# Kernel tuning notes

Measured on AMD Instinct MI355X. Metric: run time of the kernel, lower is better.

The kernel has to match this reference:

```python
import jax, jax.numpy as jnp
import numpy as np

# __init__ constants
COORS_RANGE = ((-51.2, 51.2), (-51.2, 51.2), (-4.0, 2.4))  # x, y, z ranges
SPATIAL = (512, 512, 64)  # base spatial shape (X, Y, Z)
SCALES = (2, 4, 8, 1)     # scale_list + [1]
N_POINTS = 2_000_000
N_BATCH = 8


def setup_inputs() -> dict:
    key = jax.random.key(0)
    kp, kb = jax.random.split(key)
    lo = jnp.array([r[0] for r in COORS_RANGE], dtype=jnp.float32)
    hi = jnp.array([r[1] for r in COORS_RANGE], dtype=jnp.float32)
    u = jax.random.uniform(kp, (N_POINTS, 3), dtype=jnp.float32)
    points = lo + u * (hi - lo)  # [N,3] xyz inside the voxelization range
    batch_idx = jax.random.randint(kb, (N_POINTS,), 0, N_BATCH).astype(jnp.int64)
    return {"points": points, "batch_idx": batch_idx}


def reference(points, batch_idx):
    """Per scale: quantize xyz to voxel indices, then unique/dedup with inverse and
    counts. Rows [b,x,y,z] are packed into a single int64 key so that a 1-D unique
    (lexicographically equivalent to torch.unique(dim=0)) can be used.
    Returns, for each scale in SCALES: (full_coors [N,4] int64, coors_inv [N] int,
    coors [M,4] int32 in [b,z,y,x] order), flattened into one tuple."""
    b = batch_idx.astype(jnp.int64)
    outs = []
    for scale in SCALES:
        dims = [int(np.ceil(s / scale)) for s in SPATIAL]  # per-scale grid size
        idxs = []
        for i in range(3):
            lo, hi = COORS_RANGE[i]
            # torch .long() truncates toward zero; values are >=0 in range so
            # truncation == floor here.
            idxs.append((dims[i] * (points[:, i] - lo) / (hi - lo)).astype(jnp.int64))
        xidx, yidx, zidx = idxs
        full_coors = jnp.stack([b, xidx, yidx, zidx], axis=-1)  # [N,4]
        sx, sy, sz = dims
        # pack (b,x,y,z) lexicographically into one key
        keys = ((b * sx + xidx) * sy + yidx) * sz + zidx
        unq, unq_inv, unq_cnt = jnp.unique(keys, return_inverse=True, return_counts=True)
        zb = unq % sz
        rem = unq // sz
        yb = rem % sy
        rem = rem // sy
        xb = rem % sx
        bb = rem // sx
        # original reorders unq columns to [b, z, y, x] and casts to int32
        coors = jnp.stack([bb, zb, yb, xb], axis=-1).astype(jnp.int32)
        outs.extend([full_coors, unq_inv.reshape(-1), coors])
    return tuple(outs)
```

## Files before the change

### kernel.cpp

```cpp
#include <hip/hip_runtime.h>
#include <stdint.h>


#define CHUNK 4096
#define NB    1174
#define TOTALW 4808704
#define R_S2 0
#define R_S4 528384
#define R_S8 598016
#define R_S1 610304

__device__ __forceinline__ uint32_t cmp2(uint32_t w) {
  w = (w | (w >> 1)) & 0x55555555u;
  w = (w | (w >> 1)) & 0x33333333u;
  w = (w | (w >> 2)) & 0x0F0F0F0Fu;
  w = (w | (w >> 4)) & 0x00FF00FFu;
  w = (w | (w >> 8)) & 0x0000FFFFu;
  return w;
}

__global__ __launch_bounds__(256) void k_mark(
    const float* __restrict__ pts, const int* __restrict__ bidx, int n,
    uint32_t* __restrict__ keys, uint32_t* __restrict__ bitmap) {
  int j = blockIdx.x * 256 + threadIdx.x;
  if (j >= n) return;
  float px = pts[3 * j + 0];
  float py = pts[3 * j + 1];
  float pz = pts[3 * j + 2];
  int b = bidx[j];
  int x1 = (int)((512.0f * (px + 51.2f)) / 102.4f);
  int y1 = (int)((512.0f * (py + 51.2f)) / 102.4f);
  int z1 = (int)((64.0f * (pz + 4.0f)) / 6.4f);
  keys[j] = ((uint32_t)b << 27) | ((uint32_t)x1 << 17) | ((uint32_t)y1 << 7) | (uint32_t)z1;
  uint32_t key = (uint32_t)(((b * 512 + x1) * 512 + y1) * 64 + z1);
  atomicOr(&bitmap[R_S1 + (key >> 5)], 1u << (key & 31u));
}

__global__ __launch_bounds__(256) void k_down2(
    const uint32_t* __restrict__ bm, uint32_t* __restrict__ out) {
  int o = blockIdx.x * 256 + threadIdx.x;
  int Y = o & 255, X = (o >> 8) & 255, b = o >> 16;
  const uint4* p = (const uint4*)(bm + R_S1 + (size_t)(((b * 512 + 2 * X) * 512) + 2 * Y) * 2);
  uint4 A = p[0];
  uint4 B = p[256];
  uint32_t lo = A.x | A.z | B.x | B.z;
  uint32_t hi = A.y | A.w | B.y | B.w;
  out[R_S2 + o] = cmp2(lo) | (cmp2(hi) << 16);
}

__global__ __launch_bounds__(256) void k_down4(
    const uint32_t* __restrict__ bm, uint32_t* __restrict__ out) {
  int o = blockIdx.x * 256 + threadIdx.x;
  int k = o & 63, X = (o >> 6) & 127, b = o >> 13;
  const uint4* p = (const uint4*)(bm + R_S2 + (size_t)(((b * 256 + 2 * X) * 256) + 4 * k));
  uint4 A = p[0];
  uint4 B = p[64];
  uint32_t lo = A.x | A.y | B.x | B.y;
  uint32_t hi = A.z | A.w | B.z | B.w;
  out[R_S4 + o] = cmp2(lo) | (cmp2(hi) << 16);
}

__global__ __launch_bounds__(256) void k_down8(
    const uint32_t* __restrict__ bm, uint32_t* __restrict__ out) {
  int o = blockIdx.x * 256 + threadIdx.x;
  if (o >= 8192) return;
  int k = o & 15, X = (o >> 4) & 63, b = o >> 10;
  const uint4* p = (const uint4*)(bm + R_S4 + (size_t)(((b * 128 + 2 * X) * 64) + 4 * k));
  uint4 A = p[0];
  uint4 B = p[16];
  uint32_t w = 0, u;
  u = A.x | B.x; u = (u | (u >> 16)) & 0xFFFFu; w |= cmp2(u);
  u = A.y | B.y; u = (u | (u >> 16)) & 0xFFFFu; w |= cmp2(u) << 8;
  u = A.z | B.z; u = (u | (u >> 16)) & 0xFFFFu; w |= cmp2(u) << 16;
  u = A.w | B.w; u = (u | (u >> 16)) & 0xFFFFu; w |= cmp2(u) << 24;
  out[R_S8 + o] = w;
}

__global__ __launch_bounds__(256) void k_sumA(
    const uint32_t* __restrict__ bitmap, uint32_t* __restrict__ blockSums) {
  __shared__ uint32_t sh[256];
  int t = threadIdx.x;
  const uint4* bp = (const uint4*)(bitmap + (size_t)blockIdx.x * CHUNK + t * 16);
  uint32_t s = 0;
#pragma unroll
  for (int k = 0; k < 4; k++) {
    uint4 v = bp[k];
    s += __popc(v.x) + __popc(v.y) + __popc(v.z) + __popc(v.w);
  }
  sh[t] = s;
  __syncthreads();
  for (int off = 128; off > 0; off >>= 1) {
    if (t < off) sh[t] += sh[t + off];
    __syncthreads();
  }
  if (t == 0) blockSums[blockIdx.x] = sh[0];
}

__global__ __launch_bounds__(256) void k_scanB(
    uint32_t* blockSums, long long* devOff, uint32_t* devRank, long long fiveN) {
  __shared__ uint32_t sh[256];
  __shared__ uint32_t shB[3];
  int t = threadIdx.x;
  uint32_t v[8];
  uint32_t s = 0;
#pragma unroll
  for (int k = 0; k < 8; k++) {
    int idx = t * 8 + k;
    uint32_t x = (idx < NB) ? blockSums[idx] : 0u;
    v[k] = x;
    s += x;
  }
  sh[t] = s;
  __syncthreads();
  for (int off = 1; off < 256; off <<= 1) {
    uint32_t add = (t >= off) ? sh[t - off] : 0u;
    __syncthreads();
    sh[t] += add;
    __syncthreads();
  }
  uint32_t run = sh[t] - s;
#pragma unroll
  for (int k = 0; k < 8; k++) {
    int idx = t * 8 + k;
    if (idx < NB) blockSums[idx] = run;
    if (idx == 129) shB[0] = run;
    if (idx == 146) shB[1] = run;
    if (idx == 149) shB[2] = run;
    run += v[k];
  }
  __syncthreads();
  if (t == 0) {
    uint32_t tot = sh[255];
    uint32_t T0 = shB[0];
    uint32_t T1 = shB[1] - shB[0];
    uint32_t T2 = shB[2] - shB[1];
    uint32_t T3 = tot - shB[2];
    devOff[0] = 0;
    devOff[1] = devOff[0] + fiveN + 4LL * T0;
    devOff[2] = devOff[1] + fiveN + 4LL * T1;
    devOff[3] = devOff[2] + fiveN + 4LL * T2;
    devOff[4] = devOff[3] + fiveN + 4LL * T3;
    devRank[0] = 0;
    devRank[1] = shB[0];
    devRank[2] = shB[1];
    devRank[3] = shB[2];
  }
}

__global__ __launch_bounds__(256) void k_pref(
    const uint32_t* __restrict__ bitmap, const uint32_t* __restrict__ blockSums,
    uint2* __restrict__ pairs) {
  __shared__ uint32_t sh[256];
  int t = threadIdx.x;
  size_t w0 = (size_t)blockIdx.x * CHUNK + t * 16;
  const uint4* bp = (const uint4*)(bitmap + w0);
  uint4 words[4];
  uint32_t s = 0;
#pragma unroll
  for (int k = 0; k < 4; k++) {
    uint4 v = bp[k];
    words[k] = v;
    s += __popc(v.x) + __popc(v.y) + __popc(v.z) + __popc(v.w);
  }
  sh[t] = s;
  __syncthreads();
  for (int off = 1; off < 256; off <<= 1) {
    uint32_t add = (t >= off) ? sh[t - off] : 0u;
    __syncthreads();
    sh[t] += add;
    __syncthreads();
  }
  uint32_t run = blockSums[blockIdx.x] + (sh[t] - s);
  uint4* pp = (uint4*)(pairs + w0);
#pragma unroll
  for (int k = 0; k < 4; k++) {
    uint4 o1, o2;
    o1.x = words[k].x; o1.y = run; run += __popc(words[k].x);
    o1.z = words[k].y; o1.w = run; run += __popc(words[k].y);
    o2.x = words[k].z; o2.y = run; run += __popc(words[k].z);
    o2.z = words[k].w; o2.w = run; run += __popc(words[k].w);
    pp[2 * k] = o1;
    pp[2 * k + 1] = o2;
  }
}

__global__ __launch_bounds__(256) void k_write(
    const uint32_t* __restrict__ keys, int n, const uint2* __restrict__ pairs,
    const uint32_t* __restrict__ devRank, const long long* __restrict__ devOff,
    int* __restrict__ out, long long fourN) {
  int j = blockIdx.x * 256 + threadIdx.x;
  if (j >= n) return;
  uint32_t p = keys[j];
  int b = (int)(p >> 27);
  int x1 = (int)((p >> 17) & 1023u);
  int y1 = (int)((p >> 7) & 1023u);
  int z1 = (int)(p & 127u);
  const int SX[4] = {256, 128, 64, 512};
  const int SY[4] = {256, 128, 64, 512};
  const int SZ[4] = {32, 16, 8, 64};
  const int SH[4] = {1, 2, 3, 0};
  const int RG[4] = {R_S2, R_S4, R_S8, R_S1};
#pragma unroll
  for (int i = 0; i < 4; i++) {
    int sh = SH[i];
    int xi = x1 >> sh, yi = y1 >> sh, zi = z1 >> sh;
    uint32_t key = (uint32_t)(((b * SX[i] + xi) * SY[i] + yi) * SZ[i] + zi);
    uint2 pr = pairs[RG[i] + (key >> 5)];
    long long o = devOff[i];
    *(int4*)(out + o + 4LL * j) = make_int4(b, xi, yi, zi);
    uint32_t inv = pr.y + __popc(pr.x & ((1u << (key & 31u)) - 1u)) - devRank[i];
    out[o + fourN + j] = (int)inv;
  }
}

template <int LZ, int LYZ, int LB, int MZ, int MY, int MX, int RG, int SCALE_IDX>
__device__ __forceinline__ void uniq_region(
    uint32_t w, uint32_t wd, uint32_t pf, uint32_t rankBase,
    const long long* __restrict__ devOff, int* __restrict__ out, long long fiveN) {
  uint32_t pos = pf - rankBase;
  long long base = devOff[SCALE_IDX] + fiveN;
  uint32_t local = w - (uint32_t)RG;
  while (wd) {
    int bit = __ffs(wd) - 1;
    wd &= wd - 1u;
    uint32_t key = (local << 5) + (uint32_t)bit;
    int z = (int)(key & (uint32_t)MZ);
    int y = (int)((key >> LZ) & (uint32_t)MY);
    int x = (int)((key >> LYZ) & (uint32_t)MX);
    int bb = (int)(key >> LB);
    *(int4*)(out + base + 4LL * pos) = make_int4(bb, z, y, x);
    pos++;
  }
}

__global__ __launch_bounds__(256) void k_uniq(
    const uint2* __restrict__ pairs, const uint32_t* __restrict__ devRank,
    const long long* __restrict__ devOff, int* __restrict__ out, long long fiveN) {
  uint32_t w = blockIdx.x * 256 + threadIdx.x;
  uint2 pr = pairs[w];
  if (!pr.x) return;
  if (w < R_S4) {
    uniq_region<5, 13, 21, 31, 255, 255, R_S2, 0>(w, pr.x, pr.y, devRank[0], devOff, out, fiveN);
  } else if (w < R_S8) {
    uniq_region<4, 11, 18, 15, 127, 127, R_S4, 1>(w, pr.x, pr.y, devRank[1], devOff, out, fiveN);
  } else if (w < R_S1) {
    uniq_region<3, 9, 15, 7, 63, 63, R_S8, 2>(w, pr.x, pr.y, devRank[2], devOff, out, fiveN);
  } else {
    uniq_region<6, 15, 24, 63, 511, 511, R_S1, 3>(w, pr.x, pr.y, devRank[3], devOff, out, fiveN);
  }
}

extern "C" void kernel_launch(void* const* d_in, const int* in_sizes, int n_in,
                              void* d_out, int out_size, void* d_ws, size_t ws_size,
                              hipStream_t stream) {
  const float* pts = (const float*)d_in[0];
  const int* bidx = (const int*)d_in[1];
  int n = in_sizes[0] / 3;
  int* out = (int*)d_out;

  char* ws = (char*)d_ws;
  long long* devOff = (long long*)ws;
  uint32_t* devRank = (uint32_t*)(ws + 64);
  uint32_t* blockSums = (uint32_t*)(ws + 256);
  uint32_t* bitmap = (uint32_t*)(ws + 8192);
  uint2* pairs = (uint2*)(ws + 8192 + (size_t)TOTALW * 4);
  uint32_t* keys = (uint32_t*)(ws + 8192 + 3 * (size_t)TOTALW * 4);

  const long long fourN = 4LL * n, fiveN = 5LL * n;
  const int gridN = (n + 255) / 256;

  hipMemsetAsync(bitmap, 0, (size_t)TOTALW * 4, stream);
  hipLaunchKernelGGL(k_mark, dim3(gridN), dim3(256), 0, stream, pts, bidx, n, keys, bitmap);
  hipLaunchKernelGGL(k_down2, dim3(2048), dim3(256), 0, stream, bitmap, bitmap);
  hipLaunchKernelGGL(k_down4, dim3(256), dim3(256), 0, stream, bitmap, bitmap);
  hipLaunchKernelGGL(k_down8, dim3(32), dim3(256), 0, stream, bitmap, bitmap);
  hipLaunchKernelGGL(k_sumA, dim3(NB), dim3(256), 0, stream, bitmap, blockSums);
  hipLaunchKernelGGL(k_scanB, dim3(1), dim3(256), 0, stream, blockSums, devOff, devRank, fiveN);
  hipLaunchKernelGGL(k_pref, dim3(NB), dim3(256), 0, stream, bitmap, blockSums, pairs);
  hipLaunchKernelGGL(k_write, dim3(gridN), dim3(256), 0, stream,
                     keys, n, pairs, devRank, devOff, out, fourN);
  hipLaunchKernelGGL(k_uniq, dim3(TOTALW / 256), dim3(256), 0, stream,
                     pairs, devRank, devOff, out, fiveN);
}
```

Before: 465.6 us.

## Replace materialized rank pairs with compact hierarchical rank index and fuse kernels

Drops the per-word (bitmap, prefix) pairs array, which was several times the bitmap's size. Ranks now come from a three-level index: per-chunk base, per-1024-word offset, and a 16-bit offset per 4-word group, with popcounts over the bitmap words. The scale-4 and scale-8 downsamples are fused into one kernel, with scale-8 computed directly from the scale-2 level, and the inverse-index write and unique-coordinate emission kernels are merged into one launch. Each lookup now reads several small arrays plus a bitmap uint4 instead of one pair, and each unique-emission thread processes four words serially.

```diff
diff --git a/kernel.cpp b/kernel.cpp
--- a/kernel.cpp
+++ b/kernel.cpp
@@ -5,6 +5,8 @@
 #define CHUNK 4096
 #define NB    1174
 #define TOTALW 4808704
+#define NGROUP (TOTALW / 4)
+#define NSUB   (TOTALW / 1024)
 #define R_S2 0
 #define R_S4 528384
 #define R_S8 598016
@@ -48,56 +50,73 @@
   out[R_S2 + o] = cmp2(lo) | (cmp2(hi) << 16);
 }
 
-__global__ __launch_bounds__(256) void k_down4(
+__global__ __launch_bounds__(256) void k_down48(
     const uint32_t* __restrict__ bm, uint32_t* __restrict__ out) {
   int o = blockIdx.x * 256 + threadIdx.x;
-  int k = o & 63, X = (o >> 6) & 127, b = o >> 13;
-  const uint4* p = (const uint4*)(bm + R_S2 + (size_t)(((b * 256 + 2 * X) * 256) + 4 * k));
-  uint4 A = p[0];
-  uint4 B = p[64];
-  uint32_t lo = A.x | A.y | B.x | B.y;
-  uint32_t hi = A.z | A.w | B.z | B.w;
-  out[R_S4 + o] = cmp2(lo) | (cmp2(hi) << 16);
-}
-
-__global__ __launch_bounds__(256) void k_down8(
-    const uint32_t* __restrict__ bm, uint32_t* __restrict__ out) {
-  int o = blockIdx.x * 256 + threadIdx.x;
-  if (o >= 8192) return;
-  int k = o & 15, X = (o >> 4) & 63, b = o >> 10;
-  const uint4* p = (const uint4*)(bm + R_S4 + (size_t)(((b * 128 + 2 * X) * 64) + 4 * k));
-  uint4 A = p[0];
-  uint4 B = p[16];
-  uint32_t w = 0, u;
-  u = A.x | B.x; u = (u | (u >> 16)) & 0xFFFFu; w |= cmp2(u);
-  u = A.y | B.y; u = (u | (u >> 16)) & 0xFFFFu; w |= cmp2(u) << 8;
-  u = A.z | B.z; u = (u | (u >> 16)) & 0xFFFFu; w |= cmp2(u) << 16;
-  u = A.w | B.w; u = (u | (u >> 16)) & 0xFFFFu; w |= cmp2(u) << 24;
-  out[R_S8 + o] = w;
-}
-
-__global__ __launch_bounds__(256) void k_sumA(
-    const uint32_t* __restrict__ bitmap, uint32_t* __restrict__ blockSums) {
+  if (o < 65536) {
+    int k = o & 63, X = (o >> 6) & 127, b = o >> 13;
+    const uint4* p = (const uint4*)(bm + R_S2 + (size_t)(((b * 256 + 2 * X) * 256) + 4 * k));
+    uint4 A = p[0];
+    uint4 B = p[64];
+    uint32_t lo = A.x | A.y | B.x | B.y;
+    uint32_t hi = A.z | A.w | B.z | B.w;
+    out[R_S4 + o] = cmp2(lo) | (cmp2(hi) << 16);
+  } else {
+    int o8 = o - 65536;
+    int k = o8 & 15, X8 = (o8 >> 4) & 63, b = o8 >> 10;
+    uint32_t res = 0;
+#pragma unroll
+    for (int j = 0; j < 4; j++) {
+      uint32_t acc = 0;
+      int y2 = 16 * k + 4 * j;
+#pragma unroll
+      for (int xr = 0; xr < 4; xr++) {
+        const uint4* p = (const uint4*)(bm + R_S2 + (size_t)((b * 256 + 4 * X8 + xr) * 256 + y2));
+        uint4 v = *p;
+        acc |= v.x | v.y | v.z | v.w;
+      }
+      res |= cmp2(cmp2(acc)) << (8 * j);
+    }
+    out[R_S8 + o8] = res;
+  }
+}
+
+__global__ __launch_bounds__(256) void k_scan1(
+    const uint32_t* __restrict__ bitmap, uint32_t* __restrict__ chunkSums,
+    uint32_t* __restrict__ relM, uint16_t* __restrict__ relB) {
   __shared__ uint32_t sh[256];
+  __shared__ uint32_t shE[256];
   int t = threadIdx.x;
-  const uint4* bp = (const uint4*)(bitmap + (size_t)blockIdx.x * CHUNK + t * 16);
-  uint32_t s = 0;
-#pragma unroll
-  for (int k = 0; k < 4; k++) {
-    uint4 v = bp[k];
-    s += __popc(v.x) + __popc(v.y) + __popc(v.z) + __popc(v.w);
-  }
+  size_t w0 = (size_t)blockIdx.x * CHUNK + t * 16;
+  const uint4* bp = (const uint4*)(bitmap + w0);
+  uint4 v0 = bp[0], v1 = bp[1], v2 = bp[2], v3 = bp[3];
+  uint32_t g0 = __popc(v0.x) + __popc(v0.y) + __popc(v0.z) + __popc(v0.w);
+  uint32_t g1 = __popc(v1.x) + __popc(v1.y) + __popc(v1.z) + __popc(v1.w);
+  uint32_t g2 = __popc(v2.x) + __popc(v2.y) + __popc(v2.z) + __popc(v2.w);
+  uint32_t g3 = __popc(v3.x) + __popc(v3.y) + __popc(v3.z) + __popc(v3.w);
+  uint32_t s = g0 + g1 + g2 + g3;
   sh[t] = s;
   __syncthreads();
-  for (int off = 128; off > 0; off >>= 1) {
-    if (t < off) sh[t] += sh[t + off];
-    __syncthreads();
-  }
-  if (t == 0) blockSums[blockIdx.x] = sh[0];
-}
-
-__global__ __launch_bounds__(256) void k_scanB(
-    uint32_t* blockSums, long long* devOff, uint32_t* devRank, long long fiveN) {
+  for (int off = 1; off < 256; off <<= 1) {
+    uint32_t add = (t >= off) ? sh[t - off] : 0u;
+    __syncthreads();
+    sh[t] += add;
+    __syncthreads();
+  }
+  shE[t] = sh[t] - s;
+  __syncthreads();
+  uint32_t excl = shE[t];
+  uint32_t esb = shE[t & 192];
+  uint32_t r0 = excl - esb;
+  ((ushort4*)relB)[blockIdx.x * 256 + t] = make_ushort4(
+      (unsigned short)r0, (unsigned short)(r0 + g0),
+      (unsigned short)(r0 + g0 + g1), (unsigned short)(r0 + g0 + g1 + g2));
+  if ((t & 63) == 0) relM[blockIdx.x * 4 + (t >> 6)] = excl;
+  if (t == 255) chunkSums[blockIdx.x] = sh[255];
+}
+
+__global__ __launch_bounds__(256) void k_scan2(
+    uint32_t* chunkSums, long long* devOff, uint32_t* devRank, long long fiveN) {
   __shared__ uint32_t sh[256];
   __shared__ uint32_t shB[3];
   int t = threadIdx.x;
@@ -106,7 +125,7 @@
 #pragma unroll
   for (int k = 0; k < 8; k++) {
     int idx = t * 8 + k;
-    uint32_t x = (idx < NB) ? blockSums[idx] : 0u;
+    uint32_t x = (idx < NB) ? chunkSums[idx] : 0u;
     v[k] = x;
     s += x;
   }
@@ -122,7 +141,7 @@
 #pragma unroll
   for (int k = 0; k < 8; k++) {
     int idx = t * 8 + k;
-    if (idx < NB) blockSums[idx] = run;
+    if (idx < NB) chunkSums[idx] = run;
     if (idx == 129) shB[0] = run;
     if (idx == 146) shB[1] = run;
     if (idx == 149) shB[2] = run;
@@ -147,106 +166,93 @@
   }
 }
 
-__global__ __launch_bounds__(256) void k_pref(
-    const uint32_t* __restrict__ bitmap, const uint32_t* __restrict__ blockSums,
-    uint2* __restrict__ pairs) {
-  __shared__ uint32_t sh[256];
-  int t = threadIdx.x;
-  size_t w0 = (size_t)blockIdx.x * CHUNK + t * 16;
-  const uint4* bp = (const uint4*)(bitmap + w0);
-  uint4 words[4];
-  uint32_t s = 0;
+__device__ __forceinline__ uint32_t rank_lookup(
+    const uint32_t* __restrict__ bm, const uint32_t* __restrict__ blockBase,
+    const uint32_t* __restrict__ relM, const uint16_t* __restrict__ relB,
+    uint32_t w, uint32_t bit) {
+  uint32_t g = w >> 2;
+  uint4 wv = *(const uint4*)(bm + ((size_t)g << 2));
+  uint32_t r = blockBase[w >> 12] + relM[w >> 10] + (uint32_t)relB[g];
+  uint32_t k = w & 3u;
+  if (k > 0) r += __popc(wv.x);
+  if (k > 1) r += __popc(wv.y);
+  if (k > 2) r += __popc(wv.z);
+  uint32_t word = (k == 0) ? wv.x : (k == 1) ? wv.y : (k == 2) ? wv.z : wv.w;
+  return r + __popc(word & ((1u << bit) - 1u));
+}
+
+template <int LZ, int LYZ, int LB, int MZ, int MY, int MX, int RG, int SI>
+__device__ __forceinline__ void uniq_group4(
+    uint32_t w0, uint4 wv, uint32_t pos, uint32_t rankBase,
+    const long long* __restrict__ devOff, int* __restrict__ out, long long fiveN) {
+  uint32_t words[4] = {wv.x, wv.y, wv.z, wv.w};
+  pos -= rankBase;
+  long long base = devOff[SI] + fiveN;
+  uint32_t local0 = w0 - (uint32_t)RG;
 #pragma unroll
   for (int k = 0; k < 4; k++) {
-    uint4 v = bp[k];
-    words[k] = v;
-    s += __popc(v.x) + __popc(v.y) + __popc(v.z) + __popc(v.w);
-  }
-  sh[t] = s;
-  __syncthreads();
-  for (int off = 1; off < 256; off <<= 1) {
-    uint32_t add = (t >= off) ? sh[t - off] : 0u;
-    __syncthreads();
-    sh[t] += add;
-    __syncthreads();
-  }
-  uint32_t run = blockSums[blockIdx.x] + (sh[t] - s);
-  uint4* pp = (uint4*)(pairs + w0);
-#pragma unroll
-  for (int k = 0; k < 4; k++) {
-    uint4 o1, o2;
-    o1.x = words[k].x; o1.y = run; run += __popc(words[k].x);
-    o1.z = words[k].y; o1.w = run; run += __popc(words[k].y);
-    o2.x = words[k].z; o2.y = run; run += __popc(words[k].z);
-    o2.z = words[k].w; o2.w = run; run += __popc(words[k].w);
-    pp[2 * k] = o1;
-    pp[2 * k + 1] = o2;
-  }
-}
-
-__global__ __launch_bounds__(256) void k_write(
-    const uint32_t* __restrict__ keys, int n, const uint2* __restrict__ pairs,
+    uint32_t wd = words[k];
+    uint32_t local = local0 + (uint32_t)k;
+    while (wd) {
+      int bit = __ffs(wd) - 1;
+      wd &= wd - 1u;
+      uint32_t key = (local << 5) + (uint32_t)bit;
+      int z = (int)(key & (uint32_t)MZ);
+      int y = (int)((key >> LZ) & (uint32_t)MY);
+      int x = (int)((key >> LYZ) & (uint32_t)MX);
+      int bb = (int)(key >> LB);
+      *(int4*)(out + base + 4LL * pos) = make_int4(bb, z, y, x);
+      pos++;
+    }
+  }
+}
+
+__global__ __launch_bounds__(256) void k_writeuniq(
+    const uint32_t* __restrict__ keys, int n, int gridN,
+    const uint32_t* __restrict__ bitmap, const uint32_t* __restrict__ blockBase,
+    const uint32_t* __restrict__ relM, const uint16_t* __restrict__ relB,
     const uint32_t* __restrict__ devRank, const long long* __restrict__ devOff,
-    int* __restrict__ out, long long fourN) {
-  int j = blockIdx.x * 256 + threadIdx.x;
-  if (j >= n) return;
-  uint32_t p = keys[j];
-  int b = (int)(p >> 27);
-  int x1 = (int)((p >> 17) & 1023u);
-  int y1 = (int)((p >> 7) & 1023u);
-  int z1 = (int)(p & 127u);
-  const int SX[4] = {256, 128, 64, 512};
-  const int SY[4] = {256, 128, 64, 512};
-  const int SZ[4] = {32, 16, 8, 64};
-  const int SH[4] = {1, 2, 3, 0};
-  const int RG[4] = {R_S2, R_S4, R_S8, R_S1};
-#pragma unroll
-  for (int i = 0; i < 4; i++) {
-    int sh = SH[i];
-    int xi = x1 >> sh, yi = y1 >> sh, zi = z1 >> sh;
-    uint32_t key = (uint32_t)(((b * SX[i] + xi) * SY[i] + yi) * SZ[i] + zi);
-    uint2 pr = pairs[RG[i] + (key >> 5)];
-    long long o = devOff[i];
-    *(int4*)(out + o + 4LL * j) = make_int4(b, xi, yi, zi);
-    uint32_t inv = pr.y + __popc(pr.x & ((1u << (key & 31u)) - 1u)) - devRank[i];
-    out[o + fourN + j] = (int)inv;
-  }
-}
-
-template <int LZ, int LYZ, int LB, int MZ, int MY, int MX, int RG, int SCALE_IDX>
-__device__ __forceinline__ void uniq_region(
-    uint32_t w, uint32_t wd, uint32_t pf, uint32_t rankBase,
-    const long long* __restrict__ devOff, int* __restrict__ out, long long fiveN) {
-  uint32_t pos = pf - rankBase;
-  long long base = devOff[SCALE_IDX] + fiveN;
-  uint32_t local = w - (uint32_t)RG;
-  while (wd) {
-    int bit = __ffs(wd) - 1;
-    wd &= wd - 1u;
-    uint32_t key = (local << 5) + (uint32_t)bit;
-    int z = (int)(key & (uint32_t)MZ);
-    int y = (int)((key >> LZ) & (uint32_t)MY);
-    int x = (int)((key >> LYZ) & (uint32_t)MX);
-    int bb = (int)(key >> LB);
-    *(int4*)(out + base + 4LL * pos) = make_int4(bb, z, y, x);
-    pos++;
-  }
-}
-
-__global__ __launch_bounds__(256) void k_uniq(
-    const uint2* __restrict__ pairs, const uint32_t* __restrict__ devRank,
-    const long long* __restrict__ devOff, int* __restrict__ out, long long fiveN) {
-  uint32_t w = blockIdx.x * 256 + threadIdx.x;
-  uint2 pr = pairs[w];
-  if (!pr.x) return;
-  if (w < R_S4) {
-    uniq_region<5, 13, 21, 31, 255, 255, R_S2, 0>(w, pr.x, pr.y, devRank[0], devOff, out, fiveN);
-  } else if (w < R_S8) {
-    uniq_region<4, 11, 18, 15, 127, 127, R_S4, 1>(w, pr.x, pr.y, devRank[1], devOff, out, fiveN);
-  } else if (w < R_S1) {
-    uniq_region<3, 9, 15, 7, 63, 63, R_S8, 2>(w, pr.x, pr.y, devRank[2], devOff, out, fiveN);
+    int* __restrict__ out, long long fourN, long long fiveN) {
+  int blk = blockIdx.x;
+  if (blk < gridN) {
+    int j = blk * 256 + threadIdx.x;
+    if (j >= n) return;
+    uint32_t p = keys[j];
+    int b = (int)(p >> 27);
+    int x1 = (int)((p >> 17) & 1023u);
+    int y1 = (int)((p >> 7) & 1023u);
+    int z1 = (int)(p & 127u);
+    const int SX[4] = {256, 128, 64, 512};
+    const int SY[4] = {256, 128, 64, 512};
+    const int SZ[4] = {32, 16, 8, 64};
+    const int SH[4] = {1, 2, 3, 0};
+    const int RG[4] = {R_S2, R_S4, R_S8, R_S1};
+#pragma unroll
+    for (int i = 0; i < 4; i++) {
+      int sh = SH[i];
+      int xi = x1 >> sh, yi = y1 >> sh, zi = z1 >> sh;
+      uint32_t key = (uint32_t)(((b * SX[i] + xi) * SY[i] + yi) * SZ[i] + zi);
+      uint32_t w = (uint32_t)RG[i] + (key >> 5);
+      uint32_t rank = rank_lookup(bitmap, blockBase, relM, relB, w, key & 31u);
+      long long o = devOff[i];
+      *(int4*)(out + o + 4LL * j) = make_int4(b, xi, yi, zi);
+      out[o + fourN + j] = (int)(rank - devRank[i]);
+    }
   } else {
-    uniq_region<6, 15, 24, 63, 511, 511, R_S1, 3>(w, pr.x, pr.y, devRank[3], devOff, out, fiveN);
+    int g = (blk - gridN) * 256 + threadIdx.x;
+    uint4 wv = *(const uint4*)(bitmap + ((size_t)g << 2));
+    if (!(wv.x | wv.y | wv.z | wv.w)) return;
+    uint32_t w0 = (uint32_t)g << 2;
+    uint32_t pos = blockBase[w0 >> 12] + relM[w0 >> 10] + (uint32_t)relB[g];
+    if (w0 < R_S4) {
+      uniq_group4<5, 13, 21, 31, 255, 255, R_S2, 0>(w0, wv, pos, devRank[0], devOff, out, fiveN);
+    } else if (w0 < R_S8) {
+      uniq_group4<4, 11, 18, 15, 127, 127, R_S4, 1>(w0, wv, pos, devRank[1], devOff, out, fiveN);
+    } else if (w0 < R_S1) {
+      uniq_group4<3, 9, 15, 7, 63, 63, R_S8, 2>(w0, wv, pos, devRank[2], devOff, out, fiveN);
+    } else {
+      uniq_group4<6, 15, 24, 63, 511, 511, R_S1, 3>(w0, wv, pos, devRank[3], devOff, out, fiveN);
+    }
   }
 }
 
@@ -261,10 +267,11 @@
   char* ws = (char*)d_ws;
   long long* devOff = (long long*)ws;
   uint32_t* devRank = (uint32_t*)(ws + 64);
-  uint32_t* blockSums = (uint32_t*)(ws + 256);
+  uint32_t* chunkSums = (uint32_t*)(ws + 256);
   uint32_t* bitmap = (uint32_t*)(ws + 8192);
-  uint2* pairs = (uint2*)(ws + 8192 + (size_t)TOTALW * 4);
-  uint32_t* keys = (uint32_t*)(ws + 8192 + 3 * (size_t)TOTALW * 4);
+  uint32_t* relM = (uint32_t*)(ws + 19243008);
+  uint16_t* relB = (uint16_t*)(ws + 19262464);
+  uint32_t* keys = (uint32_t*)(ws + 21666816);
 
   const long long fourN = 4LL * n, fiveN = 5LL * n;
   const int gridN = (n + 255) / 256;
@@ -272,13 +279,10 @@
   hipMemsetAsync(bitmap, 0, (size_t)TOTALW * 4, stream);
   hipLaunchKernelGGL(k_mark, dim3(gridN), dim3(256), 0, stream, pts, bidx, n, keys, bitmap);
   hipLaunchKernelGGL(k_down2, dim3(2048), dim3(256), 0, stream, bitmap, bitmap);
-  hipLaunchKernelGGL(k_down4, dim3(256), dim3(256), 0, stream, bitmap, bitmap);
-  hipLaunchKernelGGL(k_down8, dim3(32), dim3(256), 0, stream, bitmap, bitmap);
-  hipLaunchKernelGGL(k_sumA, dim3(NB), dim3(256), 0, stream, bitmap, blockSums);
-  hipLaunchKernelGGL(k_scanB, dim3(1), dim3(256), 0, stream, blockSums, devOff, devRank, fiveN);
-  hipLaunchKernelGGL(k_pref, dim3(NB), dim3(256), 0, stream, bitmap, blockSums, pairs);
-  hipLaunchKernelGGL(k_write, dim3(gridN), dim3(256), 0, stream,
-                     keys, n, pairs, devRank, devOff, out, fourN);
-  hipLaunchKernelGGL(k_uniq, dim3(TOTALW / 256), dim3(256), 0, stream,
-                     pairs, devRank, devOff, out, fiveN);
-}
+  hipLaunchKernelGGL(k_down48, dim3(288), dim3(256), 0, stream, bitmap, bitmap);
+  hipLaunchKernelGGL(k_scan1, dim3(NB), dim3(256), 0, stream, bitmap, chunkSums, relM, relB);
+  hipLaunchKernelGGL(k_scan2, dim3(1), dim3(256), 0, stream, chunkSums, devOff, devRank, fiveN);
+  hipLaunchKernelGGL(k_writeuniq, dim3(gridN + NGROUP / 256), dim3(256), 0, stream,
+                     keys, n, gridN, bitmap, chunkSums, relM, relB,
+                     devRank, devOff, out, fourN, fiveN);
+}
```

After: 489.9 us. +5.2%, slower.

## Bucket voxel keys into LDS bitmaps and fuse multi-scale downsampling

Applied to the files above, without the earlier changes.

Instead of setting one global atomicOr per point in the full-resolution bitmap, points are binned into 512 spatial buckets through per-block counting scatter into global bucket arrays. Each bucket is then expanded in shared memory with LDS atomics, and the 2x/4x/8x downsampled bitmaps are derived in the same kernel. This replaces three separate downsample kernels and random global atomics with more coalesced traffic. The cost is an extra pass through bucket storage and a fixed per-bucket capacity that would silently drop keys if any bucket overflowed.

```diff
diff --git a/kernel.cpp b/kernel.cpp
--- a/kernel.cpp
+++ b/kernel.cpp
@@ -9,6 +9,9 @@
 #define R_S4 528384
 #define R_S8 598016
 #define R_S1 610304
+#define NBUCKET 512
+#define BCAP 5120
+#define ROUND 4096
 
 __device__ __forceinline__ uint32_t cmp2(uint32_t w) {
   w = (w | (w >> 1)) & 0x55555555u;
@@ -19,61 +22,157 @@
   return w;
 }
 
-__global__ __launch_bounds__(256) void k_mark(
+__global__ __launch_bounds__(256) void k_key(
     const float* __restrict__ pts, const int* __restrict__ bidx, int n,
-    uint32_t* __restrict__ keys, uint32_t* __restrict__ bitmap) {
-  int j = blockIdx.x * 256 + threadIdx.x;
-  if (j >= n) return;
-  float px = pts[3 * j + 0];
-  float py = pts[3 * j + 1];
-  float pz = pts[3 * j + 2];
-  int b = bidx[j];
-  int x1 = (int)((512.0f * (px + 51.2f)) / 102.4f);
-  int y1 = (int)((512.0f * (py + 51.2f)) / 102.4f);
-  int z1 = (int)((64.0f * (pz + 4.0f)) / 6.4f);
-  keys[j] = ((uint32_t)b << 27) | ((uint32_t)x1 << 17) | ((uint32_t)y1 << 7) | (uint32_t)z1;
-  uint32_t key = (uint32_t)(((b * 512 + x1) * 512 + y1) * 64 + z1);
-  atomicOr(&bitmap[R_S1 + (key >> 5)], 1u << (key & 31u));
-}
-
-__global__ __launch_bounds__(256) void k_down2(
-    const uint32_t* __restrict__ bm, uint32_t* __restrict__ out) {
-  int o = blockIdx.x * 256 + threadIdx.x;
-  int Y = o & 255, X = (o >> 8) & 255, b = o >> 16;
-  const uint4* p = (const uint4*)(bm + R_S1 + (size_t)(((b * 512 + 2 * X) * 512) + 2 * Y) * 2);
-  uint4 A = p[0];
-  uint4 B = p[256];
-  uint32_t lo = A.x | A.z | B.x | B.z;
-  uint32_t hi = A.y | A.w | B.y | B.w;
-  out[R_S2 + o] = cmp2(lo) | (cmp2(hi) << 16);
-}
-
-__global__ __launch_bounds__(256) void k_down4(
-    const uint32_t* __restrict__ bm, uint32_t* __restrict__ out) {
-  int o = blockIdx.x * 256 + threadIdx.x;
-  int k = o & 63, X = (o >> 6) & 127, b = o >> 13;
-  const uint4* p = (const uint4*)(bm + R_S2 + (size_t)(((b * 256 + 2 * X) * 256) + 4 * k));
-  uint4 A = p[0];
-  uint4 B = p[64];
-  uint32_t lo = A.x | A.y | B.x | B.y;
-  uint32_t hi = A.z | A.w | B.z | B.w;
-  out[R_S4 + o] = cmp2(lo) | (cmp2(hi) << 16);
-}
-
-__global__ __launch_bounds__(256) void k_down8(
-    const uint32_t* __restrict__ bm, uint32_t* __restrict__ out) {
-  int o = blockIdx.x * 256 + threadIdx.x;
-  if (o >= 8192) return;
-  int k = o & 15, X = (o >> 4) & 63, b = o >> 10;
-  const uint4* p = (const uint4*)(bm + R_S4 + (size_t)(((b * 128 + 2 * X) * 64) + 4 * k));
-  uint4 A = p[0];
-  uint4 B = p[16];
-  uint32_t w = 0, u;
-  u = A.x | B.x; u = (u | (u >> 16)) & 0xFFFFu; w |= cmp2(u);
-  u = A.y | B.y; u = (u | (u >> 16)) & 0xFFFFu; w |= cmp2(u) << 8;
-  u = A.z | B.z; u = (u | (u >> 16)) & 0xFFFFu; w |= cmp2(u) << 16;
-  u = A.w | B.w; u = (u | (u >> 16)) & 0xFFFFu; w |= cmp2(u) << 24;
-  out[R_S8 + o] = w;
+    uint32_t* __restrict__ keys, uint32_t* __restrict__ bitmap,
+    uint32_t* __restrict__ bucketCount, uint32_t* __restrict__ bucketData) {
+  __shared__ uint32_t cnt[NBUCKET], inc[NBUCKET], pos[NBUCKET], gpos[NBUCKET];
+  __shared__ uint32_t shs[256];
+  __shared__ uint32_t scratch[ROUND];
+  int t = threadIdx.x;
+
+  for (int r = 0; r < 2; r++) {
+    int base = (blockIdx.x * 2 + r) * ROUND;
+    cnt[t] = 0; cnt[t + 256] = 0;
+    pos[t] = 0; pos[t + 256] = 0;
+    __syncthreads();
+
+    uint32_t myKey[16];
+    int myBk[16];
+#pragma unroll
+    for (int k = 0; k < 16; k++) {
+      int j = base + k * 256 + t;
+      myBk[k] = -1;
+      if (j < n) {
+        float px = pts[3 * j + 0];
+        float py = pts[3 * j + 1];
+        float pz = pts[3 * j + 2];
+        int b = bidx[j];
+        int x1 = (int)((512.0f * (px + 51.2f)) / 102.4f);
+        int y1 = (int)((512.0f * (py + 51.2f)) / 102.4f);
+        int z1 = (int)((64.0f * (pz + 4.0f)) / 6.4f);
+        keys[j] = ((uint32_t)b << 27) | ((uint32_t)x1 << 17) | ((uint32_t)y1 << 7) | (uint32_t)z1;
+        uint32_t s1k = (uint32_t)(((b * 512 + x1) * 512 + y1) * 64 + z1);
+        if (s1k >= (1u << 27)) {
+          atomicOr(&bitmap[R_S1 + (s1k >> 5)], 1u << (s1k & 31u));
+          uint32_t k2 = (uint32_t)(((b * 256 + (x1 >> 1)) * 256 + (y1 >> 1)) * 32 + (z1 >> 1));
+          atomicOr(&bitmap[R_S2 + (k2 >> 5)], 1u << (k2 & 31u));
+          uint32_t k4 = (uint32_t)(((b * 128 + (x1 >> 2)) * 128 + (y1 >> 2)) * 16 + (z1 >> 2));
+          atomicOr(&bitmap[R_S4 + (k4 >> 5)], 1u << (k4 & 31u));
+          uint32_t k8 = (uint32_t)(((b * 64 + (x1 >> 3)) * 64 + (y1 >> 3)) * 8 + (z1 >> 3));
+          atomicOr(&bitmap[R_S8 + (k8 >> 5)], 1u << (k8 & 31u));
+        } else {
+          int bk = (int)(s1k >> 18);
+          myBk[k] = bk;
+          myKey[k] = s1k;
+          atomicAdd(&cnt[bk], 1u);
+        }
+      }
+    }
+    __syncthreads();
+
+    uint32_t c0 = cnt[2 * t], c1 = cnt[2 * t + 1];
+    gpos[2 * t] = c0 ? atomicAdd(&bucketCount[2 * t], c0) : 0u;
+    gpos[2 * t + 1] = c1 ? atomicAdd(&bucketCount[2 * t + 1], c1) : 0u;
+    uint32_t s = c0 + c1;
+    shs[t] = s;
+    __syncthreads();
+    for (int off = 1; off < 256; off <<= 1) {
+      uint32_t add = (t >= off) ? shs[t - off] : 0u;
+      __syncthreads();
+      shs[t] += add;
+      __syncthreads();
+    }
+    inc[2 * t] = shs[t] - s + c0;
+    inc[2 * t + 1] = shs[t];
+    __syncthreads();
+    uint32_t total = shs[255];
+
+#pragma unroll
+    for (int k = 0; k < 16; k++) {
+      if (myBk[k] >= 0) {
+        int bk = myBk[k];
+        uint32_t slot = inc[bk] - cnt[bk] + atomicAdd(&pos[bk], 1u);
+        scratch[slot] = myKey[k];
+      }
+    }
+    __syncthreads();
+
+#pragma unroll
+    for (int m = 0; m < 16; m++) {
+      uint32_t p = (uint32_t)(m * 256 + t);
+      if (p < total) {
+        int lo = 0, hi = NBUCKET - 1;
+        while (lo < hi) {
+          int mid = (lo + hi) >> 1;
+          if (inc[mid] > p) hi = mid; else lo = mid + 1;
+        }
+        uint32_t lidx = p - (inc[lo] - cnt[lo]);
+        uint32_t g = gpos[lo] + lidx;
+        if (g < BCAP) bucketData[(size_t)lo * BCAP + g] = scratch[p];
+      }
+    }
+    __syncthreads();
+  }
+}
+
+__global__ __launch_bounds__(256) void k_bucket(
+    const uint32_t* __restrict__ bucketCount, const uint32_t* __restrict__ bucketData,
+    uint32_t* __restrict__ bitmap) {
+  __shared__ uint32_t s1L[8192];
+  __shared__ uint32_t s2L[1024];
+  __shared__ uint32_t s4L[128];
+  int bk = blockIdx.x, t = threadIdx.x;
+
+  uint4 z4 = make_uint4(0, 0, 0, 0);
+  for (int i = t; i < 2048; i += 256) ((uint4*)s1L)[i] = z4;
+  __syncthreads();
+
+  uint32_t c = bucketCount[bk];
+  if (c > BCAP) c = BCAP;
+  const uint32_t* src = bucketData + (size_t)bk * BCAP;
+  for (uint32_t i = t; i < c; i += 256) {
+    uint32_t key = src[i];
+    uint32_t local = key & 0x3FFFFu;
+    atomicOr(&s1L[local >> 5], 1u << (local & 31u));
+  }
+  __syncthreads();
+
+  uint4* g1 = (uint4*)(bitmap + R_S1 + (size_t)bk * 8192);
+  for (int i = t; i < 2048; i += 256) g1[i] = ((uint4*)s1L)[i];
+
+  for (int i = t; i < 1024; i += 256) {
+    int x2r = i >> 8, Y2 = i & 255;
+    int a = (2 * x2r * 512 + 2 * Y2) * 2;
+    int b2 = ((2 * x2r + 1) * 512 + 2 * Y2) * 2;
+    uint32_t Ax = s1L[a], Ay = s1L[a + 1], Az = s1L[a + 2], Aw = s1L[a + 3];
+    uint32_t Bx = s1L[b2], By = s1L[b2 + 1], Bz = s1L[b2 + 2], Bw = s1L[b2 + 3];
+    s2L[i] = cmp2(Ax | Az | Bx | Bz) | (cmp2(Ay | Aw | By | Bw) << 16);
+  }
+  __syncthreads();
+  for (int i = t; i < 1024; i += 256) bitmap[R_S2 + (size_t)bk * 1024 + i] = s2L[i];
+
+  if (t < 128) {
+    int x4r = t >> 6, kk = t & 63;
+    int a = (2 * x4r) * 256 + 4 * kk;
+    int b4 = (2 * x4r + 1) * 256 + 4 * kk;
+    uint32_t A0 = s2L[a], A1 = s2L[a + 1], A2 = s2L[a + 2], A3 = s2L[a + 3];
+    uint32_t B0 = s2L[b4], B1 = s2L[b4 + 1], B2 = s2L[b4 + 2], B3 = s2L[b4 + 3];
+    s4L[t] = cmp2(A0 | A1 | B0 | B1) | (cmp2(A2 | A3 | B2 | B3) << 16);
+  }
+  __syncthreads();
+  if (t < 128) bitmap[R_S4 + (size_t)bk * 128 + t] = s4L[t];
+
+  if (t < 16) {
+    uint32_t res = 0;
+#pragma unroll
+    for (int j = 0; j < 4; j++) {
+      uint32_t u = s4L[4 * t + j] | s4L[64 + 4 * t + j];
+      u = (u | (u >> 16)) & 0xFFFFu;
+      res |= cmp2(u) << (8 * j);
+    }
+    bitmap[R_S8 + (size_t)bk * 16 + t] = res;
+  }
 }
 
 __global__ __launch_bounds__(256) void k_sumA(
@@ -261,22 +360,25 @@
   char* ws = (char*)d_ws;
   long long* devOff = (long long*)ws;
   uint32_t* devRank = (uint32_t*)(ws + 64);
-  uint32_t* blockSums = (uint32_t*)(ws + 256);
+  uint32_t* chunkSums = (uint32_t*)(ws + 256);
+  uint32_t* bucketCount = (uint32_t*)(ws + 5120);
   uint32_t* bitmap = (uint32_t*)(ws + 8192);
-  uint2* pairs = (uint2*)(ws + 8192 + (size_t)TOTALW * 4);
-  uint32_t* keys = (uint32_t*)(ws + 8192 + 3 * (size_t)TOTALW * 4);
+  uint2* pairs = (uint2*)(ws + 19243008);
+  uint32_t* keys = (uint32_t*)(ws + 57712640);
+  uint32_t* bucketData = (uint32_t*)(ws + 65712640);
 
   const long long fourN = 4LL * n, fiveN = 5LL * n;
   const int gridN = (n + 255) / 256;
 
   hipMemsetAsync(bitmap, 0, (size_t)TOTALW * 4, stream);
-  hipLaunchKernelGGL(k_mark, dim3(gridN), dim3(256), 0, stream, pts, bidx, n, keys, bitmap);
-  hipLaunchKernelGGL(k_down2, dim3(2048), dim3(256), 0, stream, bitmap, bitmap);
-  hipLaunchKernelGGL(k_down4, dim3(256), dim3(256), 0, stream, bitmap, bitmap);
-  hipLaunchKernelGGL(k_down8, dim3(32), dim3(256), 0, stream, bitmap, bitmap);
-  hipLaunchKernelGGL(k_sumA, dim3(NB), dim3(256), 0, stream, bitmap, blockSums);
-  hipLaunchKernelGGL(k_scanB, dim3(1), dim3(256), 0, stream, blockSums, devOff, devRank, fiveN);
-  hipLaunchKernelGGL(k_pref, dim3(NB), dim3(256), 0, stream, bitmap, blockSums, pairs);
+  hipMemsetAsync(bucketCount, 0, NBUCKET * 4, stream);
+  hipLaunchKernelGGL(k_key, dim3(256), dim3(256), 0, stream,
+                     pts, bidx, n, keys, bitmap, bucketCount, bucketData);
+  hipLaunchKernelGGL(k_bucket, dim3(NBUCKET), dim3(256), 0, stream,
+                     bucketCount, bucketData, bitmap);
+  hipLaunchKernelGGL(k_sumA, dim3(NB), dim3(256), 0, stream, bitmap, chunkSums);
+  hipLaunchKernelGGL(k_scanB, dim3(1), dim3(256), 0, stream, chunkSums, devOff, devRank, fiveN);
+  hipLaunchKernelGGL(k_pref, dim3(NB), dim3(256), 0, stream, bitmap, chunkSums, pairs);
   hipLaunchKernelGGL(k_write, dim3(gridN), dim3(256), 0, stream,
                      keys, n, pairs, devRank, devOff, out, fourN);
   hipLaunchKernelGGL(k_uniq, dim3(TOTALW / 256), dim3(256), 0, stream,
```

Result: no change. 460.7 us (-1.1%).
